# Kernel optimization log

Measured on AMD Instinct MI355X. Metric: run time of the kernel, lower is better.

The kernel has to match this reference:

```python
import jax, jax.numpy as jnp
import numpy as np

H = 100  # hidden_state

def _lstm(x, W_ih, W_hh, b_ih, b_hh):
    # x: [B, T, D]; PyTorch gate order: i, f, g, o
    B, T, D = x.shape
    xg = jnp.einsum('btd,gd->btg', x, W_ih) + b_ih + b_hh  # [B, T, 4H]
    xg = jnp.transpose(xg, (1, 0, 2))  # [T, B, 4H]

    def step(carry, xt):
        h, c = carry
        g = xt + h @ W_hh.T
        i = jax.nn.sigmoid(g[:, 0*H:1*H])
        f = jax.nn.sigmoid(g[:, 1*H:2*H])
        gg = jnp.tanh(g[:, 2*H:3*H])
        o = jax.nn.sigmoid(g[:, 3*H:4*H])
        c = f * c + i * gg
        h = o * jnp.tanh(c)
        return (h, c), h

    h0 = jnp.zeros((B, H), x.dtype)
    c0 = jnp.zeros((B, H), x.dtype)
    _, hs = jax.lax.scan(step, (h0, c0), xg)  # [T, B, H]
    return jnp.transpose(hs, (1, 0, 2))  # [B, T, H]

def setup_inputs() -> dict:
    key = jax.random.key(0)
    ks = jax.random.split(key, 12)
    B, T, D, F = 64, 2048, 128, 300
    s = 1.0 / np.sqrt(H)
    u = lambda k, shape, sc: jax.random.uniform(k, shape, jnp.float32, -sc, sc)
    return {
        'x': jax.random.normal(ks[0], (B, T, D), jnp.float32),
        'y': jax.random.normal(ks[1], (B, T, D), jnp.float32),
        'W_ih': u(ks[2], (4 * H, D), s),
        'W_hh': u(ks[3], (4 * H, H), s),
        'b_ih': u(ks[4], (4 * H,), s),
        'b_hh': u(ks[5], (4 * H,), s),
        'ff1_w': u(ks[6], (F, H), 1.0 / np.sqrt(H)),
        'ff1_b': u(ks[7], (F,), 1.0 / np.sqrt(H)),
        'ff2_w': u(ks[8], (D, F), 1.0 / np.sqrt(F)),
        'ff2_b': u(ks[9], (D,), 1.0 / np.sqrt(F)),
    }

def reference(x, y, W_ih, W_hh, b_ih, b_hh, ff1_w, ff1_b, ff2_w, ff2_b):
    out = _lstm(x, W_ih, W_hh, b_ih, b_hh)          # [B, T, H]
    out = jax.nn.relu(out)
    out = jax.nn.relu(out @ ff1_w.T + ff1_b)         # [B, T, F]
    out = out @ ff2_w.T + ff2_b                      # [B, T, D]
    # training-mode forward returns out (e only updates running sigma stats)
    return out
```

## Files before the change

kernel.cpp:

```cpp
#include <hip/hip_runtime.h>
#include <math.h>

constexpr int H_ = 100;
constexpr int D_ = 128;
constexpr int F_ = 300;
constexpr int T_ = 2048;
constexpr int B_ = 64;
constexpr int G_ = 4 * H_;

static __device__ __forceinline__ float fast_rcp(float x) {
    return __builtin_amdgcn_rcpf(x);
}
static __device__ __forceinline__ float sigmoid_f(float g) {
    return fast_rcp(1.f + __expf(-g));
}
static __device__ __forceinline__ float tanh_f(float g) {
    float gg = fminf(fmaxf(g, -15.f), 15.f);
    float e = __expf(2.f * gg);
    return (e - 1.f) * fast_rcp(e + 1.f);
}

constexpr int AROWS = 32;

__global__ __launch_bounds__(512, 2) void xg_gemm(
    const float* __restrict__ x, const float* __restrict__ W_ih,
    const float* __restrict__ b_ih, const float* __restrict__ b_hh,
    float* __restrict__ xg)
{
    __shared__ float xs[AROWS * D_];
    const int tid = threadIdx.x;
    const long rowbase = (long)blockIdx.x * AROWS;

    {
        const float4* gx = (const float4*)(x + rowbase * D_);
        float4* sx = (float4*)xs;
        for (int i = tid; i < AROWS * D_ / 4; i += 512) sx[i] = gx[i];
    }
    __syncthreads();

    if (tid < G_) {
        float w[D_];
        const float4* wp = (const float4*)(W_ih + tid * D_);
        #pragma unroll
        for (int k4 = 0; k4 < D_ / 4; ++k4) {
            float4 v = wp[k4];
            w[4*k4+0] = v.x; w[4*k4+1] = v.y; w[4*k4+2] = v.z; w[4*k4+3] = v.w;
        }
        const float bias = b_ih[tid] + b_hh[tid];

        #pragma unroll 1
        for (int g = 0; g < AROWS / 4; ++g) {
            float a0 = bias, a1 = bias, a2 = bias, a3 = bias;
            const float4* r0 = (const float4*)&xs[(4*g + 0) * D_];
            const float4* r1 = (const float4*)&xs[(4*g + 1) * D_];
            const float4* r2 = (const float4*)&xs[(4*g + 2) * D_];
            const float4* r3 = (const float4*)&xs[(4*g + 3) * D_];
            #pragma unroll 8
            for (int k4 = 0; k4 < D_ / 4; ++k4) {
                float4 v0 = r0[k4], v1 = r1[k4], v2 = r2[k4], v3 = r3[k4];
                a0 = fmaf(w[4*k4+0], v0.x, a0); a0 = fmaf(w[4*k4+1], v0.y, a0);
                a0 = fmaf(w[4*k4+2], v0.z, a0); a0 = fmaf(w[4*k4+3], v0.w, a0);
                a1 = fmaf(w[4*k4+0], v1.x, a1); a1 = fmaf(w[4*k4+1], v1.y, a1);
                a1 = fmaf(w[4*k4+2], v1.z, a1); a1 = fmaf(w[4*k4+3], v1.w, a1);
                a2 = fmaf(w[4*k4+0], v2.x, a2); a2 = fmaf(w[4*k4+1], v2.y, a2);
                a2 = fmaf(w[4*k4+2], v2.z, a2); a2 = fmaf(w[4*k4+3], v2.w, a2);
                a3 = fmaf(w[4*k4+0], v3.x, a3); a3 = fmaf(w[4*k4+1], v3.y, a3);
                a3 = fmaf(w[4*k4+2], v3.z, a3); a3 = fmaf(w[4*k4+3], v3.w, a3);
            }
            float* orow = xg + (rowbase + 4*g) * G_ + tid;
            orow[0 * G_] = a0; orow[1 * G_] = a1;
            orow[2 * G_] = a2; orow[3 * G_] = a3;
        }
    }
}

__global__ __launch_bounds__(512, 2) void lstm_rec(
    const float* __restrict__ xg,
    const float* __restrict__ W_hh,
    float* __restrict__ hout)
{
    __shared__ float h_lds[H_];
    __shared__ float a_lds[G_];
    const int j = threadIdx.x;
    const int b = blockIdx.x;
    const float* xgb = xg + (long)b * T_ * G_;
    float* hb = hout + (long)b * T_ * H_;

    float w[H_];
    if (j < G_) {
        const float4* wp = (const float4*)(W_hh + j * H_);
        #pragma unroll
        for (int k4 = 0; k4 < H_ / 4; ++k4) {
            float4 v = wp[k4];
            w[4*k4+0] = v.x; w[4*k4+1] = v.y; w[4*k4+2] = v.z; w[4*k4+3] = v.w;
        }
    }
    if (j < H_) h_lds[j] = 0.f;
    float c = 0.f;

    float xg_c = (j < G_) ? xgb[j] : 0.f;
    float xg_n = (j < G_) ? xgb[G_ + j] : 0.f;
    __syncthreads();

    #define LSTM_STEP(XGV, TIDX)                                             \
    {                                                                        \
        if (j < G_) {                                                        \
            float a0 = (XGV), a1 = 0.f, a2 = 0.f, a3 = 0.f;                  \
            _Pragma("unroll")                                                \
            for (int k4 = 0; k4 < H_ / 4; ++k4) {                            \
                float4 hv = *(const float4*)&h_lds[4 * k4];                  \
                a0 = fmaf(w[4*k4+0], hv.x, a0);                              \
                a1 = fmaf(w[4*k4+1], hv.y, a1);                              \
                a2 = fmaf(w[4*k4+2], hv.z, a2);                              \
                a3 = fmaf(w[4*k4+3], hv.w, a3);                              \
            }                                                                \
            float gv = (a0 + a1) + (a2 + a3);                                \
            float act;                                                       \
            if (j < 2 * H_ || j >= 3 * H_) act = sigmoid_f(gv);              \
            else                            act = tanh_f(gv);                \
            a_lds[j] = act;                                                  \
        }                                                                    \
        __syncthreads();                                                     \
        if (j < H_) {                                                        \
            float ig = a_lds[j], fg = a_lds[H_ + j];                         \
            float gg = a_lds[2 * H_ + j], og = a_lds[3 * H_ + j];            \
            c = fmaf(fg, c, ig * gg);                                        \
            float hv = og * tanh_f(c);                                       \
            h_lds[j] = hv;                                                   \
            hb[(long)(TIDX) * H_ + j] = hv;                                  \
        }                                                                    \
        __syncthreads();                                                     \
    }

    for (int t = 0; t < T_; t += 2) {
        float p0 = (j < G_ && t + 2 < T_) ? xgb[(long)(t + 2) * G_ + j] : 0.f;
        float p1 = (j < G_ && t + 3 < T_) ? xgb[(long)(t + 3) * G_ + j] : 0.f;
        LSTM_STEP(xg_c, t);
        LSTM_STEP(xg_n, t + 1);
        xg_c = p0; xg_n = p1;
    }
    #undef LSTM_STEP
}

constexpr int CROWS = 32;

__global__ __launch_bounds__(512, 2) void ffn(
    const float* __restrict__ hin,
    const float* __restrict__ ff1_w, const float* __restrict__ ff1_b,
    const float* __restrict__ ff2_w, const float* __restrict__ ff2_b,
    float* __restrict__ out)
{
    __shared__ float hs[CROWS * H_];
    __shared__ float fs[CROWS * F_];
    const int tid = threadIdx.x;
    const long rowbase = (long)blockIdx.x * CROWS;

    {
        const float4* gh = (const float4*)(hin + rowbase * H_);
        float4* sh = (float4*)hs;
        for (int i = tid; i < CROWS * H_ / 4; i += 512) {
            float4 v = gh[i];
            v.x = fmaxf(v.x, 0.f); v.y = fmaxf(v.y, 0.f);
            v.z = fmaxf(v.z, 0.f); v.w = fmaxf(v.w, 0.f);
            sh[i] = v;
        }
    }
    __syncthreads();

    if (tid < F_) {
        float w[H_];
        const float4* wp = (const float4*)(ff1_w + tid * H_);
        #pragma unroll
        for (int k4 = 0; k4 < H_ / 4; ++k4) {
            float4 v = wp[k4];
            w[4*k4+0] = v.x; w[4*k4+1] = v.y; w[4*k4+2] = v.z; w[4*k4+3] = v.w;
        }
        const float bias = ff1_b[tid];
        #pragma unroll 1
        for (int g = 0; g < CROWS / 4; ++g) {
            float a0 = bias, a1 = bias, a2 = bias, a3 = bias;
            const float4* r0 = (const float4*)&hs[(4*g + 0) * H_];
            const float4* r1 = (const float4*)&hs[(4*g + 1) * H_];
            const float4* r2 = (const float4*)&hs[(4*g + 2) * H_];
            const float4* r3 = (const float4*)&hs[(4*g + 3) * H_];
            #pragma unroll
            for (int k4 = 0; k4 < H_ / 4; ++k4) {
                float4 v0 = r0[k4], v1 = r1[k4], v2 = r2[k4], v3 = r3[k4];
                a0 = fmaf(w[4*k4+0], v0.x, a0); a0 = fmaf(w[4*k4+1], v0.y, a0);
                a0 = fmaf(w[4*k4+2], v0.z, a0); a0 = fmaf(w[4*k4+3], v0.w, a0);
                a1 = fmaf(w[4*k4+0], v1.x, a1); a1 = fmaf(w[4*k4+1], v1.y, a1);
                a1 = fmaf(w[4*k4+2], v1.z, a1); a1 = fmaf(w[4*k4+3], v1.w, a1);
                a2 = fmaf(w[4*k4+0], v2.x, a2); a2 = fmaf(w[4*k4+1], v2.y, a2);
                a2 = fmaf(w[4*k4+2], v2.z, a2); a2 = fmaf(w[4*k4+3], v2.w, a2);
                a3 = fmaf(w[4*k4+0], v3.x, a3); a3 = fmaf(w[4*k4+1], v3.y, a3);
                a3 = fmaf(w[4*k4+2], v3.z, a3); a3 = fmaf(w[4*k4+3], v3.w, a3);
            }
            fs[(4*g + 0) * F_ + tid] = fmaxf(a0, 0.f);
            fs[(4*g + 1) * F_ + tid] = fmaxf(a1, 0.f);
            fs[(4*g + 2) * F_ + tid] = fmaxf(a2, 0.f);
            fs[(4*g + 3) * F_ + tid] = fmaxf(a3, 0.f);
        }
    }
    __syncthreads();

    {
        const int col = tid & (D_ - 1);
        const int rg  = tid >> 7;
        const float4* wp = (const float4*)(ff2_w + col * F_);
        const float bias = ff2_b[col];
        float acc[8];
        #pragma unroll
        for (int r = 0; r < 8; ++r) acc[r] = bias;

        #pragma unroll 5
        for (int k4 = 0; k4 < F_ / 4; ++k4) {
            float4 wv = wp[k4];
            #pragma unroll
            for (int r = 0; r < 8; ++r) {
                const float4 v = *(const float4*)&fs[(rg * 8 + r) * F_ + 4 * k4];
                acc[r] = fmaf(wv.x, v.x, acc[r]);
                acc[r] = fmaf(wv.y, v.y, acc[r]);
                acc[r] = fmaf(wv.z, v.z, acc[r]);
                acc[r] = fmaf(wv.w, v.w, acc[r]);
            }
        }
        #pragma unroll
        for (int r = 0; r < 8; ++r)
            out[(rowbase + rg * 8 + r) * D_ + col] = acc[r];
    }
}

extern "C" void kernel_launch(void* const* d_in, const int* in_sizes, int n_in,
                              void* d_out, int out_size, void* d_ws, size_t ws_size,
                              hipStream_t stream) {
    const float* x     = (const float*)d_in[0];
    const float* W_ih  = (const float*)d_in[2];
    const float* W_hh  = (const float*)d_in[3];
    const float* b_ih  = (const float*)d_in[4];
    const float* b_hh  = (const float*)d_in[5];
    const float* ff1_w = (const float*)d_in[6];
    const float* ff1_b = (const float*)d_in[7];
    const float* ff2_w = (const float*)d_in[8];
    const float* ff2_b = (const float*)d_in[9];
    float* out = (float*)d_out;

    float* xg   = (float*)d_ws;
    float* hbuf = xg + (long)B_ * T_ * G_;

    xg_gemm<<<(B_ * T_) / AROWS, 512, 0, stream>>>(x, W_ih, b_ih, b_hh, xg);
    lstm_rec<<<B_, 512, 0, stream>>>(xg, W_hh, hbuf);
    ffn<<<(B_ * T_) / CROWS, 512, 0, stream>>>(hbuf, ff1_w, ff1_b, ff2_w, ff2_b, out);
}
```

Measured before the change: 3.640 ms.

## Restructure LSTM recurrence with wave-shuffle gate exchange and double-buffered h

The recurrent kernel now maps the four gates of each hidden unit to lanes 16 apart within one wave. It gathers i/f/g/o with xor shuffles instead of writing them to shared memory, which removes one of the two barriers per timestep. The hidden state is double-buffered in LDS, the per-step barrier is a raw s_barrier, and tanh is computed through the sigmoid to drop the clamp. The ff2 weights are also pre-permuted so global loads in the FFN coalesce, and asm keep-alive hints are added on the weight loads. The cost is 448 threads (7 waves) with redundant clamped lanes and an extra prep kernel launch.

```diff
diff --git a/kernel.cpp b/kernel.cpp
--- a/kernel.cpp
+++ b/kernel.cpp
@@ -8,16 +8,16 @@
 constexpr int B_ = 64;
 constexpr int G_ = 4 * H_;
 
+#define KEEP4(v) asm volatile("" : "+v"(v.x), "+v"(v.y), "+v"(v.z), "+v"(v.w))
+
 static __device__ __forceinline__ float fast_rcp(float x) {
     return __builtin_amdgcn_rcpf(x);
 }
-static __device__ __forceinline__ float sigmoid_f(float g) {
-    return fast_rcp(1.f + __expf(-g));
-}
-static __device__ __forceinline__ float tanh_f(float g) {
-    float gg = fminf(fmaxf(g, -15.f), 15.f);
-    float e = __expf(2.f * gg);
-    return (e - 1.f) * fast_rcp(e + 1.f);
+static __device__ __forceinline__ float sigmoid_f(float u) {
+    return fast_rcp(1.f + __expf(-u));
+}
+static __device__ __forceinline__ float tanh_safe(float c) {
+    return fmaf(-2.f, fast_rcp(__expf(2.f * c) + 1.f), 1.f);
 }
 
 constexpr int AROWS = 32;
@@ -44,6 +44,7 @@
         #pragma unroll
         for (int k4 = 0; k4 < D_ / 4; ++k4) {
             float4 v = wp[k4];
+            KEEP4(v);
             w[4*k4+0] = v.x; w[4*k4+1] = v.y; w[4*k4+2] = v.z; w[4*k4+3] = v.w;
         }
         const float bias = b_ih[tid] + b_hh[tid];
@@ -74,72 +75,98 @@
     }
 }
 
-__global__ __launch_bounds__(512, 2) void lstm_rec(
+__global__ __launch_bounds__(448, 1) void lstm_rec(
     const float* __restrict__ xg,
     const float* __restrict__ W_hh,
     float* __restrict__ hout)
 {
-    __shared__ float h_lds[H_];
-    __shared__ float a_lds[G_];
-    const int j = threadIdx.x;
-    const int b = blockIdx.x;
-    const float* xgb = xg + (long)b * T_ * G_;
-    float* hb = hout + (long)b * T_ * H_;
+    __shared__ float h_lds[2][128];
+    const int tid  = threadIdx.x;
+    const int lane = tid & 63;
+    const int wv   = tid >> 6;
+    const int g0   = lane >> 4;
+    const int eo   = lane & 15;
+    const int e    = wv * 16 + eo;
+    const int ec   = (e < H_) ? e : (H_ - 1);
+    const bool writer = (g0 == 0) && (e < H_);
+    const int j    = g0 * H_ + ec;
+    const float* xgb = xg + (long)blockIdx.x * T_ * G_ + j;
+    float* hb = hout + (long)blockIdx.x * T_ * H_;
 
     float w[H_];
-    if (j < G_) {
+    {
         const float4* wp = (const float4*)(W_hh + j * H_);
         #pragma unroll
         for (int k4 = 0; k4 < H_ / 4; ++k4) {
             float4 v = wp[k4];
+            KEEP4(v);
             w[4*k4+0] = v.x; w[4*k4+1] = v.y; w[4*k4+2] = v.z; w[4*k4+3] = v.w;
         }
     }
-    if (j < H_) h_lds[j] = 0.f;
+    if (tid < H_) h_lds[0][tid] = 0.f;
     float c = 0.f;
-
-    float xg_c = (j < G_) ? xgb[j] : 0.f;
-    float xg_n = (j < G_) ? xgb[G_ + j] : 0.f;
-    __syncthreads();
-
-    #define LSTM_STEP(XGV, TIDX)                                             \
+    const bool isg = (g0 == 2);
+    const bool sw0 = (g0 & 1) != 0;
+    const bool sw1 = (g0 & 2) != 0;
+
+    float p0 = xgb[0 * G_], p1 = xgb[1 * G_], p2 = xgb[2 * G_], p3 = xgb[3 * G_];
+    __syncthreads();
+
+#define STEP(PV, TIDX, RB, WB)                                               \
     {                                                                        \
-        if (j < G_) {                                                        \
-            float a0 = (XGV), a1 = 0.f, a2 = 0.f, a3 = 0.f;                  \
-            _Pragma("unroll")                                                \
-            for (int k4 = 0; k4 < H_ / 4; ++k4) {                            \
-                float4 hv = *(const float4*)&h_lds[4 * k4];                  \
-                a0 = fmaf(w[4*k4+0], hv.x, a0);                              \
-                a1 = fmaf(w[4*k4+1], hv.y, a1);                              \
-                a2 = fmaf(w[4*k4+2], hv.z, a2);                              \
-                a3 = fmaf(w[4*k4+3], hv.w, a3);                              \
-            }                                                                \
-            float gv = (a0 + a1) + (a2 + a3);                                \
-            float act;                                                       \
-            if (j < 2 * H_ || j >= 3 * H_) act = sigmoid_f(gv);              \
-            else                            act = tanh_f(gv);                \
-            a_lds[j] = act;                                                  \
+        float a0 = (PV), a1 = 0.f, a2 = 0.f, a3 = 0.f;                       \
+        _Pragma("unroll")                                                    \
+        for (int k4 = 0; k4 < H_ / 4; ++k4) {                                \
+            float4 hv = *(const float4*)&h_lds[RB][4 * k4];                  \
+            a0 = fmaf(w[4*k4+0], hv.x, a0);                                  \
+            a1 = fmaf(w[4*k4+1], hv.y, a1);                                  \
+            a2 = fmaf(w[4*k4+2], hv.z, a2);                                  \
+            a3 = fmaf(w[4*k4+3], hv.w, a3);                                  \
         }                                                                    \
-        __syncthreads();                                                     \
-        if (j < H_) {                                                        \
-            float ig = a_lds[j], fg = a_lds[H_ + j];                         \
-            float gg = a_lds[2 * H_ + j], og = a_lds[3 * H_ + j];            \
-            c = fmaf(fg, c, ig * gg);                                        \
-            float hv = og * tanh_f(c);                                       \
-            h_lds[j] = hv;                                                   \
-            hb[(long)(TIDX) * H_ + j] = hv;                                  \
+        float gv  = (a0 + a1) + (a2 + a3);                                   \
+        float uu  = isg ? 2.f * gv : gv;                                     \
+        float sg  = sigmoid_f(uu);                                           \
+        float act = isg ? fmaf(2.f, sg, -1.f) : sg;     \
+        float q1 = __shfl_xor(act, 16, 64);                                  \
+        float q2 = __shfl_xor(act, 32, 64);                                  \
+        float q3 = __shfl_xor(act, 48, 64);                                  \
+           \
+        float t0 = sw0 ? q1 : act, t1 = sw0 ? act : q1;                      \
+        float t2 = sw0 ? q3 : q2,  t3 = sw0 ? q2 : q3;                       \
+        float gi = sw1 ? t2 : t0,  gf = sw1 ? t3 : t1;                       \
+        float gG = sw1 ? t0 : t2,  go = sw1 ? t1 : t3;                       \
+        c = fmaf(gf, c, gi * gG);                                            \
+        float hv2 = go * tanh_safe(c);                                       \
+        if (writer) {                                                        \
+            h_lds[WB][e] = hv2;                                              \
+            hb[(TIDX) * H_ + e] = hv2;                                       \
         }                                                                    \
-        __syncthreads();                                                     \
-    }
-
-    for (int t = 0; t < T_; t += 2) {
-        float p0 = (j < G_ && t + 2 < T_) ? xgb[(long)(t + 2) * G_ + j] : 0.f;
-        float p1 = (j < G_ && t + 3 < T_) ? xgb[(long)(t + 3) * G_ + j] : 0.f;
-        LSTM_STEP(xg_c, t);
-        LSTM_STEP(xg_n, t + 1);
-        xg_c = p0; xg_n = p1;
-    }
-    #undef LSTM_STEP
+        asm volatile("s_waitcnt lgkmcnt(0)" ::: "memory");                   \
+        __builtin_amdgcn_s_barrier();                                        \
+        asm volatile("" ::: "memory");                                       \
+    }
+
+    for (int t = 0; t < T_; t += 4) {
+        float n0 = (t + 4 < T_) ? xgb[(t + 4) * G_] : 0.f;
+        float n1 = (t + 5 < T_) ? xgb[(t + 5) * G_] : 0.f;
+        float n2 = (t + 6 < T_) ? xgb[(t + 6) * G_] : 0.f;
+        float n3 = (t + 7 < T_) ? xgb[(t + 7) * G_] : 0.f;
+        STEP(p0, t + 0, 0, 1);
+        STEP(p1, t + 1, 1, 0);
+        STEP(p2, t + 2, 0, 1);
+        STEP(p3, t + 3, 1, 0);
+        p0 = n0; p1 = n1; p2 = n2; p3 = n3;
+    }
+#undef STEP
+}
+
+__global__ void prep_ff2(const float* __restrict__ ff2_w,
+                         float* __restrict__ ff2_wP) {
+    int i = blockIdx.x * 256 + threadIdx.x;
+    if (i < D_ * F_) {
+        int col = i / F_, k = i % F_;
+        ff2_wP[((k >> 2) * D_ + col) * 4 + (k & 3)] = ff2_w[i];
+    }
 }
 
 constexpr int CROWS = 32;
@@ -147,7 +174,7 @@
 __global__ __launch_bounds__(512, 2) void ffn(
     const float* __restrict__ hin,
     const float* __restrict__ ff1_w, const float* __restrict__ ff1_b,
-    const float* __restrict__ ff2_w, const float* __restrict__ ff2_b,
+    const float* __restrict__ ff2_wP, const float* __restrict__ ff2_b,
     float* __restrict__ out)
 {
     __shared__ float hs[CROWS * H_];
@@ -173,6 +200,7 @@
         #pragma unroll
         for (int k4 = 0; k4 < H_ / 4; ++k4) {
             float4 v = wp[k4];
+            KEEP4(v);
             w[4*k4+0] = v.x; w[4*k4+1] = v.y; w[4*k4+2] = v.z; w[4*k4+3] = v.w;
         }
         const float bias = ff1_b[tid];
@@ -206,7 +234,7 @@
     {
         const int col = tid & (D_ - 1);
         const int rg  = tid >> 7;
-        const float4* wp = (const float4*)(ff2_w + col * F_);
+        const float4* wq = (const float4*)ff2_wP;
         const float bias = ff2_b[col];
         float acc[8];
         #pragma unroll
@@ -214,7 +242,7 @@
 
         #pragma unroll 5
         for (int k4 = 0; k4 < F_ / 4; ++k4) {
-            float4 wv = wp[k4];
+            float4 wv = wq[k4 * D_ + col];
             #pragma unroll
             for (int r = 0; r < 8; ++r) {
                 const float4 v = *(const float4*)&fs[(rg * 8 + r) * F_ + 4 * k4];
@@ -244,10 +272,12 @@
     const float* ff2_b = (const float*)d_in[9];
     float* out = (float*)d_out;
 
-    float* xg   = (float*)d_ws;
-    float* hbuf = xg + (long)B_ * T_ * G_;
-
+    float* xg    = (float*)d_ws;
+    float* hbuf  = xg + (long)B_ * T_ * G_;
+    float* ff2wp = hbuf + (long)B_ * T_ * H_;
+
+    prep_ff2<<<(D_ * F_ + 255) / 256, 256, 0, stream>>>(ff2_w, ff2wp);
     xg_gemm<<<(B_ * T_) / AROWS, 512, 0, stream>>>(x, W_ih, b_ih, b_hh, xg);
-    lstm_rec<<<B_, 512, 0, stream>>>(xg, W_hh, hbuf);
-    ffn<<<(B_ * T_) / CROWS, 512, 0, stream>>>(hbuf, ff1_w, ff1_b, ff2_w, ff2_b, out);
-}
+    lstm_rec<<<B_, 448, 0, stream>>>(xg, W_hh, hbuf);
+    ffn<<<(B_ * T_) / CROWS, 512, 0, stream>>>(hbuf, ff1_w, ff1_b, ff2wp, ff2_b, out);
+}
```

Measured after the change: 4.037 ms. 1.11x slower.
